# Performance work log

Hardware: AMD Instinct MI355X
Metric: run time of the kernel (lower is better)

Reference implementation:

```python
import jax, jax.numpy as jnp
import numpy as np
from jax import lax

B, T, D, H, W = 2, 8, 64, 64, 64
E, HID = 4, 256


def _layernorm(x, g, b, eps=1e-5):
    m = x.mean(-1, keepdims=True)
    v = ((x - m) ** 2).mean(-1, keepdims=True)
    return (x - m) / jnp.sqrt(v + eps) * g + b


def _pscan(A, X, axis):
    # linear recurrence h_t = A_t * h_{t-1} + X_t via associative scan
    def comb(l, r):
        a1, x1 = l
        a2, x2 = r
        return a2 * a1, a2 * x1 + x2
    return lax.associative_scan(comb, (A, X), axis=axis)[1]


def setup_inputs() -> dict:
    key = jax.random.key(0)
    ks = jax.random.split(key, 32)
    r = lambda i, shape, s=1.0: jax.random.normal(ks[i], shape, jnp.float32) * s
    D2 = 2 * D
    return {
        'x_re': r(0, (B, T, D, H, W)), 'x_im': r(1, (B, T, D, H, W)),
        'dt': jax.random.uniform(ks[2], (T,), jnp.float32, 0.5, 1.0),
        'ln_s_g': jnp.ones(D2), 'ln_s_b': jnp.zeros(D2),
        'conv_w': r(3, (3, 3, D2, D2), 0.03), 'conv_b': jnp.zeros(D2),
        'mom_w': r(4, (D2, D2), 0.08), 'mom_b': jnp.zeros(D2),
        'adv_w': jnp.full((1,), 0.1, jnp.float32),
        'enc_re': r(5, (D, D), 0.1), 'enc_im': r(6, (D, D), 0.1),
        'dec_re': r(7, (D, D), 0.1), 'dec_im': r(8, (D, D), 0.1),
        'flux_a_re': r(9, (D,)), 'flux_a_im': r(10, (D,), 0.1),
        'fin_re': r(11, (D, D), 0.1), 'fin_im': r(12, (D, D), 0.1),
        'fproj_re': r(13, (D, D), 0.1), 'fproj_im': r(14, (D, D), 0.1),
        'gate_w': r(15, (D2, D), 0.1), 'gate_b': jnp.zeros(D),
        'lam_re': r(16, (D,)), 'lam_im': r(17, (D,), 0.1),
        'noise_re': r(18, (B, T, H, W, D)), 'noise_im': r(19, (B, T, H, W, D)),
        'e_scale': jnp.full((1,), 0.1, jnp.float32),
        'ln_t_g': jnp.ones(D2), 'ln_t_b': jnp.zeros(D2),
        'router_w': r(20, (D2, E), 0.1), 'router_b': jnp.zeros(E),
        'w1': r(21, (E, D2, HID), 0.08), 'b1': jnp.zeros((E, HID)),
        'w2': r(22, (E, HID, D2), 0.08), 'b2': jnp.zeros((E, D2)),
    }


def _forward(x_re, x_im, dt, ln_s_g, ln_s_b, conv_w, conv_b, mom_w, mom_b, adv_w,
             enc_re, enc_im, dec_re, dec_im, flux_a_re, flux_a_im, fin_re, fin_im,
             fproj_re, fproj_im, gate_w, gate_b, lam_re, lam_im, noise_re, noise_im,
             e_scale, ln_t_g, ln_t_b, router_w, router_b, w1, b1, w2, b2):
    x = (x_re + 1j * x_im).astype(jnp.complex64)            # [B,T,D,H,W]
    target_energy = (jnp.abs(x) ** 2).mean(axis=(-2, -1))   # [B,T,D]
    momentum = x.mean(axis=(-2, -1))                        # [B,T,D] complex
    xcl = jnp.transpose(x, (0, 1, 3, 4, 2))                 # [B,T,H,W,D]
    Bs, Ts, Hs, Ws, Ds = xcl.shape
    D2 = 2 * Ds
    # --- spatial complex (Clifford) conv branch: LN over 2D channels + conv ---
    xr = jnp.concatenate([xcl.real, xcl.imag], -1)          # [B,T,H,W,2D]
    xn = _layernorm(xr, ln_s_g, ln_s_b)
    y = lax.conv_general_dilated(xn.reshape(Bs * Ts, Hs, Ws, D2), conv_w,
                                 (1, 1), 'SAME',
                                 dimension_numbers=('NHWC', 'HWIO', 'NHWC')) + conv_b
    y = y.reshape(Bs, Ts, Hs, Ws, D2)
    xcl = xcl + (y[..., :Ds] + 1j * y[..., Ds:])
    # --- momentum advection ---
    z_mean = xcl.mean(axis=(2, 3))                          # [B,T,D]
    mom_cat = jnp.concatenate([momentum.real, momentum.imag], -1) @ mom_w + mom_b
    mom_new = mom_cat[..., :Ds] + 1j * mom_cat[..., Ds:]
    dtb = jnp.broadcast_to(dt[None, :], (Bs, Ts))
    xcl = xcl + (mom_new * adv_w[0])[:, :, None, None, :] * dtb[:, :, None, None, None]
    momentum = 0.9 * momentum + 0.1 * z_mean
    # --- eigenbasis encode ---
    x_eigen = xcl @ (enc_re + 1j * enc_im)                  # [B,T,H,W,D]
    x_mean = x_eigen.mean(axis=(2, 3))                      # [B,T,D]
    # --- flux tracker: parallel scan over T ---
    A_flux = jnp.exp(-jax.nn.softplus(flux_a_re) + 1j * flux_a_im)
    A_flux = jnp.broadcast_to(A_flux, (Bs, Ts, Ds)).astype(jnp.complex64)
    X_flux = x_mean @ (fin_re + 1j * fin_im)
    flux_seq = _pscan(A_flux, X_flux, axis=1)               # [B,T,D]
    source = flux_seq @ (fproj_re + 1j * fproj_im)
    gate = jax.nn.sigmoid(jnp.concatenate([flux_seq.real, flux_seq.imag], -1) @ gate_w + gate_b)
    g = gate[:, :, None, None, :]
    forcing = x_eigen * g + source[:, :, None, None, :] * (1.0 - g)
    # --- temporal propagation: per-site parallel scan over T ---
    lam = -jax.nn.softplus(lam_re) + 1j * lam_im            # [D]
    op_decay = jnp.exp(lam[None, None, :] * dtb[:, :, None])  # [B,T,D]
    op_forcing = (op_decay - 1.0) / lam
    u_t = forcing * op_forcing[:, :, None, None, :]
    A_time = jnp.broadcast_to(op_decay[:, :, None, None, :], u_t.shape)
    u_out = _pscan(A_time, u_t, axis=1)                     # [B,T,H,W,D]
    noise = 0.01 * jnp.sqrt(dtb)[:, :, None, None, None] * (noise_re + 1j * noise_im)
    u_out = u_out + noise
    # --- decode + energy projection ---
    x_out = u_out @ (dec_re + 1j * dec_im)                  # [B,T,H,W,D]
    cur_e = (jnp.abs(x_out) ** 2).mean(axis=(2, 3))
    ratio = jnp.clip(target_energy / (cur_e + 1e-8), 0.5, 2.0)
    sf = jnp.sqrt(ratio)[:, :, None, None, :]
    x_out = x_out * (1.0 + e_scale[0] * (sf - 1.0))
    # --- temporal LN + MoE FFN on real-concat tokens ---
    xr2 = jnp.concatenate([x_out.real, x_out.imag], -1)
    xn2 = _layernorm(xr2, ln_t_g, ln_t_b)                   # [B,T,H,W,2D]
    tok = xn2.reshape(-1, D2)                               # [N,2D]
    p = jax.nn.softmax(tok @ router_w + router_b, -1)       # [N,E]
    hmid = jax.nn.gelu(jnp.einsum('nd,edh->neh', tok, w1) + b1)
    eout = jnp.einsum('neh,ehd->ned', hmid, w2) + b2
    out_tok = tok + jnp.einsum('ne,ned->nd', p, eout)
    out = out_tok.reshape(Bs, Ts, Hs, Ws, D2)
    x_out_c = out[..., :Ds] + 1j * out[..., Ds:]
    z_out = xcl + x_out_c
    z = jnp.transpose(z_out, (0, 1, 4, 2, 3))               # [B,T,D,H,W]
    return jnp.stack([z.real, z.imag])                      # [2,B,T,D,H,W]


def reference(x_re, x_im, dt, ln_s_g, ln_s_b, conv_w, conv_b, mom_w, mom_b, adv_w,
              enc_re, enc_im, dec_re, dec_im, flux_a_re, flux_a_im, fin_re, fin_im,
              fproj_re, fproj_im, gate_w, gate_b, lam_re, lam_im, noise_re, noise_im,
              e_scale, ln_t_g, ln_t_b, router_w, router_b, w1, b1, w2, b2):
    return _forward(x_re, x_im, dt, ln_s_g, ln_s_b, conv_w, conv_b, mom_w, mom_b, adv_w,
                    enc_re, enc_im, dec_re, dec_im, flux_a_re, flux_a_im, fin_re, fin_im,
                    fproj_re, fproj_im, gate_w, gate_b, lam_re, lam_im, noise_re, noise_im,
                    e_scale, ln_t_g, ln_t_b, router_w, router_b, w1, b1, w2, b2)
```

## Files before the change

### kernel.cpp

```cpp
#include <hip/hip_runtime.h>
#include <hip/hip_bf16.h>
#include <math.h>


#define W_XCL_RE 0u
#define W_XCL_IM 4194304u
#define W_C      8388608u
#define W_CWT    12582912u
#define W_W1T    14680064u
#define W_W2T    14745600u
#define W_ENCM   14811136u
#define W_DECM   14819328u
#define W_XMP_RE 14827520u
#define W_XMP_IM 14893056u
#define W_EP_RE  14958592u
#define W_EP_IM  15220736u
#define W_EIG_RE 16777216u
#define W_EIG_IM 20971520u
#define W_K1R    16777216u
#define W_K1I    16842752u
#define W_K1E    16908288u
#define W_SMALL  25165824u
#define W_TE     (W_SMALL+0u)
#define W_MOMRE  (W_SMALL+1024u)
#define W_MOMIM  (W_SMALL+2048u)
#define W_MTRE   (W_SMALL+3072u)
#define W_MTIM   (W_SMALL+4096u)
#define W_GATE   (W_SMALL+5120u)
#define W_SRCRE  (W_SMALL+6144u)
#define W_SRCIM  (W_SMALL+7168u)
#define W_OPFRE  (W_SMALL+8192u)
#define W_OPFIM  (W_SMALL+9216u)
#define W_OPDRE  (W_SMALL+10240u)
#define W_OPDIM  (W_SMALL+11264u)
#define W_SCALE  (W_SMALL+12288u)

typedef __attribute__((ext_vector_type(8))) short bf16x8;
typedef __attribute__((ext_vector_type(4))) float f32x4;

__device__ __forceinline__ unsigned short bfr(float x) {
  __hip_bfloat16 h = __float2bfloat16(x);
  return *(unsigned short*)&h;
}
__device__ __forceinline__ unsigned int pk2(float a, float b) {
  return ((unsigned int)bfr(b) << 16) | (unsigned int)bfr(a);
}

__global__ __launch_bounds__(256) void k2_transpose_ln(
    const float* __restrict__ xre, const float* __restrict__ xim,
    const float* __restrict__ g, const float* __restrict__ bb_, float* ws) {
  int blk = blockIdx.x; int bt = blk >> 6, h = blk & 63;
  __shared__ float tre[64][65], tim[64][65];
  __shared__ float ps[4][64], pq[4][64], pe[4][64];
  __shared__ float mean_l[64], rstd_l[64];
  size_t inbase = (size_t)bt * 262144 + (size_t)h * 64;
  for (int i = threadIdx.x; i < 1024; i += 256) {
    int d = i >> 4, w4 = (i & 15) * 4;
    float4 vr = *(const float4*)&xre[inbase + (size_t)d * 4096 + w4];
    float4 vi = *(const float4*)&xim[inbase + (size_t)d * 4096 + w4];
    tre[d][w4] = vr.x; tre[d][w4 + 1] = vr.y; tre[d][w4 + 2] = vr.z; tre[d][w4 + 3] = vr.w;
    tim[d][w4] = vi.x; tim[d][w4 + 1] = vi.y; tim[d][w4 + 2] = vi.z; tim[d][w4 + 3] = vi.w;
  }
  __syncthreads();
  {
    int w = threadIdx.x & 63, part = threadIdx.x >> 6;
    float s = 0.f, sq = 0.f;
    for (int dd = part * 16; dd < part * 16 + 16; dd++) {
      float vr = tre[dd][w], vi = tim[dd][w];
      s += vr + vi; sq += vr * vr + vi * vi;
    }
    ps[part][w] = s; pq[part][w] = sq;
  }
  __syncthreads();
  if (threadIdx.x < 64) {
    int w = threadIdx.x;
    float s  = ps[0][w] + ps[1][w] + ps[2][w] + ps[3][w];
    float sq = pq[0][w] + pq[1][w] + pq[2][w] + pq[3][w];
    float m = s / 128.f;
    float v = sq / 128.f - m * m;
    mean_l[w] = m; rstd_l[w] = rsqrtf(v + 1e-5f);
  }
  __syncthreads();
  {
    int d = threadIdx.x & 63, part = threadIdx.x >> 6;
    float sr = 0.f, si = 0.f, se = 0.f;
    for (int w = part * 16; w < part * 16 + 16; w++) {
      float vr = tre[d][w], vi = tim[d][w];
      sr += vr; si += vi; se += vr * vr + vi * vi;
    }
    ps[part][d] = sr; pq[part][d] = si; pe[part][d] = se;
  }
  __syncthreads();
  if (threadIdx.x < 64) {
    int d = threadIdx.x;
    int idx = h * 1024 + bt * 64 + d;
    ws[W_K1R + idx] = ps[0][d] + ps[1][d] + ps[2][d] + ps[3][d];
    ws[W_K1I + idx] = pq[0][d] + pq[1][d] + pq[2][d] + pq[3][d];
    ws[W_K1E + idx] = pe[0][d] + pe[1][d] + pe[2][d] + pe[3][d];
  }
  size_t tokbase = (size_t)blk * 64;
  for (int i = threadIdx.x; i < 1024; i += 256) {
    int w = i >> 4, d4 = (i & 15) * 4;
    float4 o, p;
    o.x = tre[d4][w]; o.y = tre[d4 + 1][w]; o.z = tre[d4 + 2][w]; o.w = tre[d4 + 3][w];
    p.x = tim[d4][w]; p.y = tim[d4 + 1][w]; p.z = tim[d4 + 2][w]; p.w = tim[d4 + 3][w];
    *(float4*)&ws[W_XCL_RE + tokbase * 64 + (size_t)w * 64 + d4] = o;
    *(float4*)&ws[W_XCL_IM + tokbase * 64 + (size_t)w * 64 + d4] = p;
  }
  __hip_bfloat16* xnb = (__hip_bfloat16*)(ws + W_C);
  int c0 = (threadIdx.x & 63) * 2, wg = threadIdx.x >> 6;
  float gc0 = g[c0], bc0 = bb_[c0], gc1 = g[c0 + 1], bc1 = bb_[c0 + 1];
  for (int pass = 0; pass < 16; pass++) {
    int w = pass * 4 + wg;
    float m = mean_l[w], rs = rstd_l[w];
    float v0 = (c0 < 64) ? tre[c0][w] : tim[c0 - 64][w];
    float v1 = (c0 + 1 < 64) ? tre[c0 + 1][w] : tim[c0 + 1 - 64][w];
    *(unsigned int*)&xnb[tokbase * 128 + (size_t)w * 128 + c0] =
        pk2((v0 - m) * rs * gc0 + bc0, (v1 - m) * rs * gc1 + bc1);
  }
}

__global__ void k1b_finish(float* ws) {
  int bt = blockIdx.x, d = threadIdx.x;
  float a = 0.f, b = 0.f, c = 0.f;
  for (int h = 0; h < 64; h++) {
    int idx = h * 1024 + bt * 64 + d;
    a += ws[W_K1R + idx]; b += ws[W_K1I + idx]; c += ws[W_K1E + idx];
  }
  ws[W_MOMRE + bt * 64 + d] = a / 4096.f;
  ws[W_MOMIM + bt * 64 + d] = b / 4096.f;
  ws[W_TE + bt * 64 + d]    = c / 4096.f;
}

__global__ void k2b_mom(const float* __restrict__ mom_w, const float* __restrict__ mom_b,
                        const float* __restrict__ adv_w, const float* __restrict__ dt, float* ws) {
  int bt = blockIdx.x; int t = bt & 7;
  __shared__ float mc[128], outl[128];
  int tid = threadIdx.x;
  mc[tid] = (tid < 64) ? ws[W_MOMRE + bt * 64 + tid] : ws[W_MOMIM + bt * 64 + tid - 64];
  __syncthreads();
  float acc = mom_b[tid];
  for (int k = 0; k < 128; k++) acc += mc[k] * mom_w[k * 128 + tid];
  outl[tid] = acc;
  __syncthreads();
  if (tid < 64) {
    float f = adv_w[0] * dt[t];
    ws[W_MTRE + bt * 64 + tid] = outl[tid] * f;
    ws[W_MTIM + bt * 64 + tid] = outl[64 + tid] * f;
  }
}

__global__ void k0_wprep(const float* __restrict__ w1, const float* __restrict__ w2,
                         const float* __restrict__ cw,
                         const float* __restrict__ enc_re, const float* __restrict__ enc_im,
                         const float* __restrict__ dec_re, const float* __restrict__ dec_im,
                         float* ws) {
  __hip_bfloat16* w1f = (__hip_bfloat16*)(ws + W_W1T);
  __hip_bfloat16* w2f = (__hip_bfloat16*)(ws + W_W2T);
  __hip_bfloat16* cwt = (__hip_bfloat16*)(ws + W_CWT);
  __hip_bfloat16* encM = (__hip_bfloat16*)(ws + W_ENCM);
  __hip_bfloat16* decM = (__hip_bfloat16*)(ws + W_DECM);
  int idx = blockIdx.x * 256 + threadIdx.x;
  if (idx < 131072) {
    {
      int j = idx & 7, lane = (idx >> 3) & 63, kt = (idx >> 9) & 3, nt = (idx >> 11) & 15, e = idx >> 15;
      int cout = nt * 16 + (lane & 15);
      int cin = kt * 32 + (lane >> 4) * 8 + j;
      w1f[idx] = __float2bfloat16(w1[((size_t)(e * 128 + cin)) * 256 + cout]);
    }
    {
      int j = idx & 7, lane = (idx >> 3) & 63, kt = (idx >> 9) & 7, nt = (idx >> 12) & 7, e = idx >> 15;
      int cout = nt * 16 + (lane & 15);
      int cin = kt * 32 + (lane >> 4) * 8 + j;
      w2f[idx] = __float2bfloat16(w2[((size_t)(e * 256 + cin)) * 128 + cout]);
    }
  }
  if (idx < 147456) {
    int j = idx & 7, lane = (idx >> 3) & 63, kt = (idx >> 9) & 3, r = idx >> 11;
    int nt = r & 7, tap = r >> 3;
    int cout = nt * 16 + (lane & 15);
    int cin = kt * 32 + (lane >> 4) * 8 + j;
    cwt[idx] = __float2bfloat16(cw[((size_t)(tap * 128 + cin)) * 128 + cout]);
  }
  if (idx < 16384) {
    int jj = idx & 7, lane = (idx >> 3) & 63, kt = (idx >> 9) & 3, nt = idx >> 11;
    int jc = nt * 16 + (lane & 15);
    int k = kt * 32 + (lane >> 4) * 8 + jj;
    float ve, vd;
    if (k < 64) {
      ve = (jc < 64) ? enc_re[k * 64 + jc] : enc_im[k * 64 + (jc - 64)];
      vd = (jc < 64) ? dec_re[k * 64 + jc] : dec_im[k * 64 + (jc - 64)];
    } else {
      int kk = k - 64;
      ve = (jc < 64) ? -enc_im[kk * 64 + jc] : enc_re[kk * 64 + (jc - 64)];
      vd = (jc < 64) ? -dec_im[kk * 64 + jc] : dec_re[kk * 64 + (jc - 64)];
    }
    encM[idx] = __float2bfloat16(ve);
    decM[idx] = __float2bfloat16(vd);
  }
}

__global__ __launch_bounds__(256) void k3_conv_enc(const float* __restrict__ cb, float* ws) {
  int blk = blockIdx.x; int bt = blk >> 6, h = blk & 63;
  const __hip_bfloat16* xnb = (const __hip_bfloat16*)(ws + W_C);
  const __hip_bfloat16* cwt = (const __hip_bfloat16*)(ws + W_CWT);
  const __hip_bfloat16* encM = (const __hip_bfloat16*)(ws + W_ENCM);
  __shared__ __align__(16) char smem[3 * 66 * 136 * 2];
  __hip_bfloat16 (*xin)[66][136] = (__hip_bfloat16(*)[66][136])smem;
  char* A = smem;
  int tid = threadIdx.x, lane = tid & 63, wv = tid >> 6;
  int arow = lane & 15, kgrp = (lane >> 4) * 8, rbase = (lane >> 4) * 4;

  for (int r = 0; r < 3; r++) {
    int hh = h + r - 1;
    if (hh < 0 || hh >= 64) {
      unsigned int* z = (unsigned int*)&xin[r][0][0];
      for (int i = tid; i < 4488; i += 256) z[i] = 0u;
    } else {
      if (tid < 68) *(unsigned int*)&xin[r][0][tid * 2] = 0u;
      else if (tid < 136) *(unsigned int*)&xin[r][65][(tid - 136 + 68) * 2] = 0u;
      const __hip_bfloat16* src = xnb + ((size_t)bt * 4096 + (size_t)hh * 64) * 128;
      for (int i = tid; i < 1024; i += 256) {
        int wp = (i >> 4) + 1, c8 = (i & 15) * 8;
        *(bf16x8*)&xin[r][wp][c8] = *(const bf16x8*)&src[(size_t)(wp - 1) * 128 + c8];
      }
    }
  }
  __syncthreads();

  f32x4 oacc[4][2];
  #pragma unroll
  for (int m = 0; m < 4; m++) {
    oacc[m][0] = (f32x4){0.f, 0.f, 0.f, 0.f};
    oacc[m][1] = (f32x4){0.f, 0.f, 0.f, 0.f};
  }

  for (int tap = 0; tap < 9; tap++) {
    int kh = tap / 3, kw = tap % 3;
    const __hip_bfloat16* wt0 = cwt + ((size_t)(tap * 8 + wv * 2) * 4) * 512 + lane * 8;
    #pragma unroll
    for (int kt = 0; kt < 4; kt++) {
      bf16x8 a[4];
      #pragma unroll
      for (int m = 0; m < 4; m++)
        a[m] = *(const bf16x8*)&xin[kh][m * 16 + arow + kw][kt * 32 + kgrp];
      bf16x8 b0 = *(const bf16x8*)&wt0[(size_t)kt * 512];
      bf16x8 b1 = *(const bf16x8*)&wt0[(size_t)(kt + 4) * 512];
      #pragma unroll
      for (int m = 0; m < 4; m++) {
        oacc[m][0] = __builtin_amdgcn_mfma_f32_16x16x32_bf16(a[m], b0, oacc[m][0], 0, 0, 0);
        oacc[m][1] = __builtin_amdgcn_mfma_f32_16x16x32_bf16(a[m], b1, oacc[m][1], 0, 0, 0);
      }
    }
  }
  __syncthreads();

  size_t rowtok = (size_t)blk * 64;
  #pragma unroll
  for (int n = 0; n < 2; n++) {
    int cout = (wv * 2 + n) * 16 + arow;
    bool isre = cout < 64;
    int d = cout & 63;
    float add = cb[cout] + ws[(isre ? W_MTRE : W_MTIM) + bt * 64 + d];
    float* xcl = ws + (isre ? W_XCL_RE : W_XCL_IM);
    #pragma unroll
    for (int m = 0; m < 4; m++)
      #pragma unroll
      for (int r = 0; r < 4; r++) {
        int w = m * 16 + rbase + r;
        float v = xcl[(rowtok + w) * 64 + d] + oacc[m][n][r] + add;
        xcl[(rowtok + w) * 64 + d] = v;
        *(__hip_bfloat16*)(A + w * 256 + ((cout * 2) ^ ((w & 7) << 4))) = __float2bfloat16(v);
      }
  }
  __syncthreads();

  f32x4 acc[4][2];
  #pragma unroll
  for (int m = 0; m < 4; m++) {
    acc[m][0] = (f32x4){0.f, 0.f, 0.f, 0.f};
    acc[m][1] = (f32x4){0.f, 0.f, 0.f, 0.f};
  }
  #pragma unroll
  for (int kt = 0; kt < 4; kt++) {
    bf16x8 a[4];
    #pragma unroll
    for (int m = 0; m < 4; m++)
      a[m] = *(const bf16x8*)(A + (m * 16 + arow) * 256 + (((kt * 32 + kgrp) * 2) ^ ((arow & 7) << 4)));
    bf16x8 b0 = *(const bf16x8*)&encM[(((size_t)(wv * 2 + 0) * 4 + kt) * 64 + lane) * 8];
    bf16x8 b1 = *(const bf16x8*)&encM[(((size_t)(wv * 2 + 1) * 4 + kt) * 64 + lane) * 8];
    #pragma unroll
    for (int m = 0; m < 4; m++) {
      acc[m][0] = __builtin_amdgcn_mfma_f32_16x16x32_bf16(a[m], b0, acc[m][0], 0, 0, 0);
      acc[m][1] = __builtin_amdgcn_mfma_f32_16x16x32_bf16(a[m], b1, acc[m][1], 0, 0, 0);
    }
  }
  float* orp = ws + W_EIG_RE;
  float* oip = ws + W_EIG_IM;
  #pragma unroll
  for (int n = 0; n < 2; n++) {
    int jc = (wv * 2 + n) * 16 + arow;
    float* dst = (jc < 64) ? orp : oip;
    int col = jc & 63;
    #pragma unroll
    for (int m = 0; m < 4; m++)
      #pragma unroll
      for (int r = 0; r < 4; r++)
        dst[(rowtok + m * 16 + rbase + r) * 64 + col] = acc[m][n][r];
    float s = 0.f;
    #pragma unroll
    for (int m = 0; m < 4; m++)
      #pragma unroll
      for (int r = 0; r < 4; r++) s += acc[m][n][r];
    s += __shfl_xor(s, 16);
    s += __shfl_xor(s, 32);
    if (lane < 16)
      ws[(jc < 64 ? W_XMP_RE : W_XMP_IM) + (size_t)blk * 64 + col] = s;
  }
}

__device__ __forceinline__ float softplusf(float x) {
  return (x > 20.f) ? x : log1pf(expf(x));
}

__global__ void k6_seq(const float* __restrict__ fin_re, const float* __restrict__ fin_im,
                       const float* __restrict__ fproj_re, const float* __restrict__ fproj_im,
                       const float* __restrict__ flux_a_re, const float* __restrict__ flux_a_im,
                       const float* __restrict__ gate_w, const float* __restrict__ gate_b,
                       const float* __restrict__ lam_re, const float* __restrict__ lam_im,
                       const float* __restrict__ dt, float* ws) {
  __shared__ float xmr[1024], xmi[1024], Xfr[1024], Xfi[1024], flr[1024], fli[1024];
  int tid = threadIdx.x;
  for (int i = tid; i < 1024; i += 256) {
    int bt = i >> 6, j = i & 63;
    float sr = 0.f, si = 0.f;
    for (int q = 0; q < 64; q++) {
      sr += ws[W_XMP_RE + (size_t)(bt * 64 + q) * 64 + j];
      si += ws[W_XMP_IM + (size_t)(bt * 64 + q) * 64 + j];
    }
    xmr[i] = sr / 4096.f; xmi[i] = si / 4096.f;
  }
  __syncthreads();
  for (int i = tid; i < 1024; i += 256) {
    int bt = i >> 6, j = i & 63;
    float ar = 0.f, ai = 0.f;
    for (int d = 0; d < 64; d++) {
      float xr = xmr[bt * 64 + d], xi = xmi[bt * 64 + d];
      float wr = fin_re[d * 64 + j], wi = fin_im[d * 64 + j];
      ar += xr * wr - xi * wi; ai += xr * wi + xi * wr;
    }
    Xfr[i] = ar; Xfi[i] = ai;
  }
  __syncthreads();
  if (tid < 128) {
    int b = tid >> 6, j = tid & 63;
    float mag = expf(-softplusf(flux_a_re[j]));
    float aar = mag * cosf(flux_a_im[j]), aai = mag * sinf(flux_a_im[j]);
    float sr = 0.f, si = 0.f;
    for (int t = 0; t < 8; t++) {
      int idx = (b * 8 + t) * 64 + j;
      float nr = aar * sr - aai * si + Xfr[idx];
      float ni = aar * si + aai * sr + Xfi[idx];
      sr = nr; si = ni;
      flr[idx] = sr; fli[idx] = si;
    }
  }
  __syncthreads();
  for (int i = tid; i < 1024; i += 256) {
    int bt = i >> 6, j = i & 63;
    float ar = 0.f, ai = 0.f, lg = 0.f;
    for (int d = 0; d < 64; d++) {
      float fr = flr[bt * 64 + d], fi = fli[bt * 64 + d];
      float wr = fproj_re[d * 64 + j], wi = fproj_im[d * 64 + j];
      ar += fr * wr - fi * wi; ai += fr * wi + fi * wr;
      lg += fr * gate_w[d * 64 + j] + fi * gate_w[(64 + d) * 64 + j];
    }
    ws[W_SRCRE + i] = ar; ws[W_SRCIM + i] = ai;
    ws[W_GATE + i] = 1.f / (1.f + expf(-(lg + gate_b[j])));
  }
  for (int i = tid; i < 1024; i += 256) {
    int bt = i >> 6, d = i & 63, t = bt & 7;
    float lr = -softplusf(lam_re[d]), li = lam_im[d];
    float dtv = dt[t];
    float mag = expf(lr * dtv);
    float dr = mag * cosf(li * dtv), di = mag * sinf(li * dtv);
    ws[W_OPDRE + i] = dr; ws[W_OPDIM + i] = di;
    float omr = dr - 1.f, omi = di;
    float den = lr * lr + li * li;
    ws[W_OPFRE + i] = (omr * lr + omi * li) / den;
    ws[W_OPFIM + i] = (omi * lr - omr * li) / den;
  }
}

__global__ __launch_bounds__(256) void k7_dec(const float* __restrict__ nre,
                                              const float* __restrict__ nim,
                                              const float* __restrict__ dt, float* ws) {
  int blk = blockIdx.x;
  int b = blk >> 8, h = (blk >> 2) & 63, wq = blk & 3;
  const __hip_bfloat16* decM = (const __hip_bfloat16*)(ws + W_DECM);
  __shared__ float gl[8][64], srl[8][64], sil[8][64], ofr[8][64], ofi[8][64], odr[8][64], odi[8][64];
  __shared__ __align__(16) char A[4096];
  __shared__ float dts[8];
  int tid = threadIdx.x, lane = tid & 63, wv = tid >> 6;
  int arow = lane & 15, kgrp = (lane >> 4) * 8, rbase = (lane >> 4) * 4;
  for (int i = tid; i < 512; i += 256) {
    int t = i >> 6, d = i & 63, idx = (b * 8 + t) * 64 + d;
    gl[t][d]  = ws[W_GATE + idx];
    srl[t][d] = ws[W_SRCRE + idx]; sil[t][d] = ws[W_SRCIM + idx];
    ofr[t][d] = ws[W_OPFRE + idx]; ofi[t][d] = ws[W_OPFIM + idx];
    odr[t][d] = ws[W_OPDRE + idx]; odi[t][d] = ws[W_OPDIM + idx];
  }
  if (tid < 8) dts[tid] = dt[tid];
  __syncthreads();

  int d = tid & 63, wbase = tid >> 6;
  float ur[4], ui[4];
  #pragma unroll
  for (int k = 0; k < 4; k++) { ur[k] = 0.f; ui[k] = 0.f; }

  for (int t = 0; t < 8; t++) {
    float ns = 0.01f * sqrtf(dts[t]);
    size_t tokb = ((size_t)(b * 8 + t) * 64 + h) * 64 + (size_t)wq * 16;
    #pragma unroll
    for (int k = 0; k < 4; k++) {
      int wl = wbase + 4 * k;
      size_t off = (tokb + wl) * 64 + d;
      float er_ = ws[W_EIG_RE + off], ei_ = ws[W_EIG_IM + off];
      float gg = gl[t][d];
      float fre = er_ * gg + srl[t][d] * (1.f - gg);
      float fim = ei_ * gg + sil[t][d] * (1.f - gg);
      float utr = fre * ofr[t][d] - fim * ofi[t][d];
      float uti = fre * ofi[t][d] + fim * ofr[t][d];
      float nur = odr[t][d] * ur[k] - odi[t][d] * ui[k] + utr;
      float nui = odr[t][d] * ui[k] + odi[t][d] * ur[k] + uti;
      ur[k] = nur; ui[k] = nui;
      float uor = nur + ns * nre[off];
      float uoi = nui + ns * nim[off];
      int sw = (wl & 7) << 4;
      *(__hip_bfloat16*)(A + wl * 256 + ((d * 2) ^ sw)) = __float2bfloat16(uor);
      *(__hip_bfloat16*)(A + wl * 256 + (((64 + d) * 2) ^ sw)) = __float2bfloat16(uoi);
    }
    __syncthreads();
    f32x4 acc[2];
    acc[0] = (f32x4){0.f, 0.f, 0.f, 0.f};
    acc[1] = (f32x4){0.f, 0.f, 0.f, 0.f};
    #pragma unroll
    for (int kt = 0; kt < 4; kt++) {
      bf16x8 a0 = *(const bf16x8*)(A + arow * 256 + (((kt * 32 + kgrp) * 2) ^ ((arow & 7) << 4)));
      bf16x8 b0 = *(const bf16x8*)&decM[(((size_t)(wv * 2 + 0) * 4 + kt) * 64 + lane) * 8];
      bf16x8 b1 = *(const bf16x8*)&decM[(((size_t)(wv * 2 + 1) * 4 + kt) * 64 + lane) * 8];
      acc[0] = __builtin_amdgcn_mfma_f32_16x16x32_bf16(a0, b0, acc[0], 0, 0, 0);
      acc[1] = __builtin_amdgcn_mfma_f32_16x16x32_bf16(a0, b1, acc[1], 0, 0, 0);
    }
    float* orp = ws + W_EIG_RE;
    float* oip = ws + W_EIG_IM;
    #pragma unroll
    for (int n = 0; n < 2; n++) {
      int jc = (wv * 2 + n) * 16 + arow;
      float* dst = (jc < 64) ? orp : oip;
      int col = jc & 63;
      #pragma unroll
      for (int r = 0; r < 4; r++)
        dst[(tokb + rbase + r) * 64 + col] = acc[n][r];
      float s = acc[n][0] * acc[n][0] + acc[n][1] * acc[n][1]
              + acc[n][2] * acc[n][2] + acc[n][3] * acc[n][3];
      s += __shfl_xor(s, 16);
      s += __shfl_xor(s, 32);
      if (lane < 16)
        ws[(jc < 64 ? W_EP_RE : W_EP_IM)
           + (size_t)((b * 8 + t) * 256 + h * 4 + wq) * 64 + col] = s;
    }
    __syncthreads();
  }
}

__global__ void k9b_scale(const float* __restrict__ escale, float* ws) {
  int bt = blockIdx.x; int j = threadIdx.x;
  float s = 0.f;
  for (int q = 0; q < 256; q++) {
    size_t idx = (size_t)(bt * 256 + q) * 64 + j;
    s += ws[W_EP_RE + idx] + ws[W_EP_IM + idx];
  }
  float cur = s / 4096.f;
  float te = ws[W_TE + bt * 64 + j];
  float ratio = te / (cur + 1e-8f);
  ratio = fminf(fmaxf(ratio, 0.5f), 2.0f);
  ws[W_SCALE + bt * 64 + j] = 1.f + escale[0] * (sqrtf(ratio) - 1.f);
}

__global__ __launch_bounds__(512) void k11_moe(
    const float* __restrict__ rw, const float* __restrict__ rb,
    const float* __restrict__ b1, const float* __restrict__ b2,
    const float* __restrict__ g2, const float* __restrict__ b2_,
    float* __restrict__ ws, float* __restrict__ out) {
  int blk = blockIdx.x; int bt = blk >> 6, h = blk & 63;
  const __hip_bfloat16* w1f = (const __hip_bfloat16*)(ws + W_W1T);
  const __hip_bfloat16* w2f = (const __hip_bfloat16*)(ws + W_W2T);
  __shared__ __align__(16) char smem[49152];
  __shared__ float pl[64][4];
  __shared__ float sc[64];
  __shared__ float mean_l[64], rstd_l[64];
  char* lt = smem;
  char* hb = smem + 16384;
  float (*obuf)[129] = (float(*)[129])smem;
  float* psq = (float*)(smem + 16384);
  int tid = threadIdx.x, lane = tid & 63, wv = tid >> 6;
  int arow = lane & 15, kgrp = (lane >> 4) * 8, rbase = (lane >> 4) * 4;
  size_t tokbase = (size_t)blk * 64;

  if (tid < 64) sc[tid] = ws[W_SCALE + bt * 64 + tid];
  __syncthreads();

  int w = tid >> 3, part = tid & 7;
  int c0 = part * 16, dbase = (part & 3) * 16;
  const float* rowp = ws + ((part < 4) ? W_EIG_RE : W_EIG_IM) + (tokbase + w) * 64 + dbase;
  float4 vv[4];
  {
    float s = 0.f, sq = 0.f;
    #pragma unroll
    for (int q = 0; q < 4; q++) {
      float4 t4 = *(const float4*)&rowp[q * 4];
      t4.x *= sc[dbase + q * 4 + 0];
      t4.y *= sc[dbase + q * 4 + 1];
      t4.z *= sc[dbase + q * 4 + 2];
      t4.w *= sc[dbase + q * 4 + 3];
      vv[q] = t4;
      s  += t4.x + t4.y + t4.z + t4.w;
      sq += t4.x * t4.x + t4.y * t4.y + t4.z * t4.z + t4.w * t4.w;
    }
    psq[part * 64 + w] = s;
    psq[512 + part * 64 + w] = sq;
  }
  __syncthreads();
  if (tid < 64) {
    float s = 0.f, sq = 0.f;
    #pragma unroll
    for (int p = 0; p < 8; p++) { s += psq[p * 64 + tid]; sq += psq[512 + p * 64 + tid]; }
    float m = s / 128.f, v = sq / 128.f - m * m;
    mean_l[tid] = m; rstd_l[tid] = rsqrtf(v + 1e-5f);
  }
  __syncthreads();
  {
    float m = mean_l[w], rs = rstd_l[w];
    int szw = (w & 7) << 4;
    #pragma unroll
    for (int q = 0; q < 4; q++) {
      int c = c0 + q * 4;
      float a0 = (vv[q].x - m) * rs * g2[c]     + b2_[c];
      float a1 = (vv[q].y - m) * rs * g2[c + 1] + b2_[c + 1];
      float a2 = (vv[q].z - m) * rs * g2[c + 2] + b2_[c + 2];
      float a3 = (vv[q].w - m) * rs * g2[c + 3] + b2_[c + 3];
      *(unsigned int*)(lt + w * 256 + ((c * 2) ^ szw)) = pk2(a0, a1);
      *(unsigned int*)(lt + w * 256 + (((c + 2) * 2) ^ szw)) = pk2(a2, a3);
    }
  }
  __syncthreads();
  if (tid < 256) {
    int l = tid >> 2, e = tid & 3;
    float acc = rb[e];
    const float* rwe = rw + e;
    int sz = (l & 7) << 4;
    for (int dd = 0; dd < 128; dd += 2) {
      unsigned int u = *(const unsigned int*)(lt + l * 256 + ((dd * 2) ^ sz));
      float x0 = __uint_as_float(u << 16);
      float x1 = __uint_as_float(u & 0xffff0000u);
      acc += x0 * rwe[dd * 4] + x1 * rwe[dd * 4 + 4];
    }
    pl[l][e] = acc;
  }
  __syncthreads();
  if (tid < 64) {
    float m = fmaxf(fmaxf(pl[tid][0], pl[tid][1]), fmaxf(pl[tid][2], pl[tid][3]));
    float e0 = expf(pl[tid][0] - m), e1 = expf(pl[tid][1] - m);
    float e2 = expf(pl[tid][2] - m), e3 = expf(pl[tid][3] - m);
    float s = e0 + e1 + e2 + e3;
    float rs = __builtin_amdgcn_rcpf(s);
    pl[tid][0] = e0 * rs; pl[tid][1] = e1 * rs; pl[tid][2] = e2 * rs; pl[tid][3] = e3 * rs;
  }

  f32x4 oacc[4];
  #pragma unroll
  for (int m = 0; m < 4; m++) {
    int col = wv * 16 + arow;
    oacc[m] = (f32x4){0.f, 0.f, 0.f, 0.f};
    #pragma unroll
    for (int r = 0; r < 4; r++) {
      int row = m * 16 + rbase + r;
      oacc[m][r] = __bfloat162float(
          *(const __hip_bfloat16*)(lt + row * 256 + ((col * 2) ^ ((row & 7) << 4))));
    }
  }
  __syncthreads();

  for (int e = 0; e < 4; e++) {
    f32x4 acc1[4][2];
    #pragma unroll
    for (int m = 0; m < 4; m++) {
      acc1[m][0] = (f32x4){0.f, 0.f, 0.f, 0.f};
      acc1[m][1] = (f32x4){0.f, 0.f, 0.f, 0.f};
    }
    #pragma unroll
    for (int kt = 0; kt < 4; kt++) {
      bf16x8 a[4];
      #pragma unroll
      for (int m = 0; m < 4; m++) {
        int row = m * 16 + arow;
        a[m] = *(const bf16x8*)(lt + row * 256 + (((kt * 32 + kgrp) * 2) ^ ((arow & 7) << 4)));
      }
      bf16x8 b0 = *(const bf16x8*)&w1f[(((size_t)(e * 16 + wv * 2 + 0) * 4 + kt) * 64 + lane) * 8];
      bf16x8 b1 = *(const bf16x8*)&w1f[(((size_t)(e * 16 + wv * 2 + 1) * 4 + kt) * 64 + lane) * 8];
      #pragma unroll
      for (int m = 0; m < 4; m++) {
        acc1[m][0] = __builtin_amdgcn_mfma_f32_16x16x32_bf16(a[m], b0, acc1[m][0], 0, 0, 0);
        acc1[m][1] = __builtin_amdgcn_mfma_f32_16x16x32_bf16(a[m], b1, acc1[m][1], 0, 0, 0);
      }
    }
    __syncthreads();
    #pragma unroll
    for (int n = 0; n < 2; n++) {
      int col = (wv * 2 + n) * 16 + arow;
      float bv = b1[e * 256 + col];
      #pragma unroll
      for (int m = 0; m < 4; m++)
        #pragma unroll
        for (int r = 0; r < 4; r++) {
          float hv = acc1[m][n][r] + bv;
          float z = 1.5957691216f * hv + 0.0713548162f * hv * hv * hv;
          float gelu = hv * __builtin_amdgcn_rcpf(1.f + __expf(-z));
          int row = m * 16 + rbase + r;
          *(__hip_bfloat16*)(hb + row * 512 + ((col * 2) ^ ((row & 7) << 4))) =
              __float2bfloat16(gelu);
        }
    }
    __syncthreads();
    f32x4 acc2[4];
    #pragma unroll
    for (int m = 0; m < 4; m++) acc2[m] = (f32x4){0.f, 0.f, 0.f, 0.f};
    #pragma unroll
    for (int kt = 0; kt < 8; kt++) {
      bf16x8 a2[4];
      #pragma unroll
      for (int m = 0; m < 4; m++) {
        int row = m * 16 + arow;
        a2[m] = *(const bf16x8*)(hb + row * 512 + (((kt * 32 + kgrp) * 2) ^ ((arow & 7) << 4)));
      }
      bf16x8 bb = *(const bf16x8*)&w2f[(((size_t)(e * 8 + wv) * 8 + kt) * 64 + lane) * 8];
      #pragma unroll
      for (int m = 0; m < 4; m++)
        acc2[m] = __builtin_amdgcn_mfma_f32_16x16x32_bf16(a2[m], bb, acc2[m], 0, 0, 0);
    }
    {
      int col = wv * 16 + arow;
      float bv2 = b2[e * 128 + col];
      #pragma unroll
      for (int m = 0; m < 4; m++)
        #pragma unroll
        for (int r = 0; r < 4; r++)
          oacc[m][r] += pl[m * 16 + rbase + r][e] * (acc2[m][r] + bv2);
    }
  }

  __syncthreads();
  #pragma unroll
  for (int m = 0; m < 4; m++) {
    int col = wv * 16 + arow;
    #pragma unroll
    for (int r = 0; r < 4; r++)
      obuf[m * 16 + rbase + r][col] = oacc[m][r];
  }
  __syncthreads();

  {
    const float* xre = ws + W_XCL_RE;
    const float* xim = ws + W_XCL_IM;
    for (int i = tid; i < 8192; i += 512) {
      int wt = i >> 7, c = i & 127, dd = c & 63;
      float val = ((c < 64) ? xre : xim)[(tokbase + wt) * 64 + dd];
      obuf[wt][c] += val;
    }
  }
  __syncthreads();
  for (int i = tid; i < 8192; i += 512) {
    int d2 = i >> 6, wt = i & 63;
    out[(size_t)(d2 >> 6) * 4194304 + (size_t)bt * 262144 + (size_t)(d2 & 63) * 4096
        + (size_t)h * 64 + wt] = obuf[wt][d2];
  }
}

extern "C" void kernel_launch(void* const* d_in, const int* in_sizes, int n_in,
                              void* d_out, int out_size, void* d_ws, size_t ws_size,
                              hipStream_t stream) {
  const float* x_re      = (const float*)d_in[0];
  const float* x_im      = (const float*)d_in[1];
  const float* dt        = (const float*)d_in[2];
  const float* ln_s_g    = (const float*)d_in[3];
  const float* ln_s_b    = (const float*)d_in[4];
  const float* conv_w    = (const float*)d_in[5];
  const float* conv_b    = (const float*)d_in[6];
  const float* mom_w     = (const float*)d_in[7];
  const float* mom_b     = (const float*)d_in[8];
  const float* adv_w     = (const float*)d_in[9];
  const float* enc_re    = (const float*)d_in[10];
  const float* enc_im    = (const float*)d_in[11];
  const float* dec_re    = (const float*)d_in[12];
  const float* dec_im    = (const float*)d_in[13];
  const float* flux_a_re = (const float*)d_in[14];
  const float* flux_a_im = (const float*)d_in[15];
  const float* fin_re    = (const float*)d_in[16];
  const float* fin_im    = (const float*)d_in[17];
  const float* fproj_re  = (const float*)d_in[18];
  const float* fproj_im  = (const float*)d_in[19];
  const float* gate_w    = (const float*)d_in[20];
  const float* gate_b    = (const float*)d_in[21];
  const float* lam_re    = (const float*)d_in[22];
  const float* lam_im    = (const float*)d_in[23];
  const float* noise_re  = (const float*)d_in[24];
  const float* noise_im  = (const float*)d_in[25];
  const float* e_scale   = (const float*)d_in[26];
  const float* ln_t_g    = (const float*)d_in[27];
  const float* ln_t_b    = (const float*)d_in[28];
  const float* router_w  = (const float*)d_in[29];
  const float* router_b  = (const float*)d_in[30];
  const float* w1        = (const float*)d_in[31];
  const float* b1        = (const float*)d_in[32];
  const float* w2        = (const float*)d_in[33];
  const float* b2        = (const float*)d_in[34];
  float* ws  = (float*)d_ws;
  float* out = (float*)d_out;

  k0_wprep<<<576, 256, 0, stream>>>(w1, w2, conv_w, enc_re, enc_im, dec_re, dec_im, ws);
  k2_transpose_ln<<<1024, 256, 0, stream>>>(x_re, x_im, ln_s_g, ln_s_b, ws);
  k1b_finish<<<16, 64, 0, stream>>>(ws);
  k2b_mom<<<16, 128, 0, stream>>>(mom_w, mom_b, adv_w, dt, ws);
  k3_conv_enc<<<1024, 256, 0, stream>>>(conv_b, ws);
  k6_seq<<<1, 256, 0, stream>>>(fin_re, fin_im, fproj_re, fproj_im, flux_a_re, flux_a_im,
                                gate_w, gate_b, lam_re, lam_im, dt, ws);
  k7_dec<<<512, 256, 0, stream>>>(noise_re, noise_im, dt, ws);
  k9b_scale<<<16, 64, 0, stream>>>(e_scale, ws);
  k11_moe<<<1024, 512, 0, stream>>>(router_w, router_b, b1, b2, ln_t_g, ln_t_b, ws, out);
}
```

Baseline: 269.4 us.

## Split MoE hidden dimension into halves to shrink LDS and vectorize epilogue I/O

The MoE kernel now computes the expert hidden layer in two 128-wide halves, running GELU and the second GEMM on each half in turn. This halves the hidden-activation LDS buffer (49152 down to 33280 bytes) and the acc1 register footprint, which should allow more blocks per CU. In exchange it adds an extra pair of barriers per expert. The residual-add and the final output store are also changed to use float4 global loads and stores.

```diff
diff --git a/kernel.cpp b/kernel.cpp
--- a/kernel.cpp
+++ b/kernel.cpp
@@ -496,7 +496,7 @@
   int blk = blockIdx.x; int bt = blk >> 6, h = blk & 63;
   const __hip_bfloat16* w1f = (const __hip_bfloat16*)(ws + W_W1T);
   const __hip_bfloat16* w2f = (const __hip_bfloat16*)(ws + W_W2T);
-  __shared__ __align__(16) char smem[49152];
+  __shared__ __align__(16) char smem[33280];
   __shared__ float pl[64][4];
   __shared__ float sc[64];
   __shared__ float mean_l[64], rstd_l[64];
@@ -593,61 +593,58 @@
   __syncthreads();
 
   for (int e = 0; e < 4; e++) {
-    f32x4 acc1[4][2];
-    #pragma unroll
-    for (int m = 0; m < 4; m++) {
-      acc1[m][0] = (f32x4){0.f, 0.f, 0.f, 0.f};
-      acc1[m][1] = (f32x4){0.f, 0.f, 0.f, 0.f};
-    }
-    #pragma unroll
-    for (int kt = 0; kt < 4; kt++) {
-      bf16x8 a[4];
-      #pragma unroll
-      for (int m = 0; m < 4; m++) {
-        int row = m * 16 + arow;
-        a[m] = *(const bf16x8*)(lt + row * 256 + (((kt * 32 + kgrp) * 2) ^ ((arow & 7) << 4)));
+    f32x4 acc2[4];
+    #pragma unroll
+    for (int m = 0; m < 4; m++) acc2[m] = (f32x4){0.f, 0.f, 0.f, 0.f};
+    #pragma unroll
+    for (int hh = 0; hh < 2; hh++) {
+      f32x4 acc1[4];
+      #pragma unroll
+      for (int m = 0; m < 4; m++) acc1[m] = (f32x4){0.f, 0.f, 0.f, 0.f};
+      #pragma unroll
+      for (int kt = 0; kt < 4; kt++) {
+        bf16x8 a[4];
+        #pragma unroll
+        for (int m = 0; m < 4; m++) {
+          int row = m * 16 + arow;
+          a[m] = *(const bf16x8*)(lt + row * 256 + (((kt * 32 + kgrp) * 2) ^ ((arow & 7) << 4)));
+        }
+        bf16x8 b0 = *(const bf16x8*)&w1f[(((size_t)(e * 16 + hh * 8 + wv) * 4 + kt) * 64 + lane) * 8];
+        #pragma unroll
+        for (int m = 0; m < 4; m++)
+          acc1[m] = __builtin_amdgcn_mfma_f32_16x16x32_bf16(a[m], b0, acc1[m], 0, 0, 0);
       }
-      bf16x8 b0 = *(const bf16x8*)&w1f[(((size_t)(e * 16 + wv * 2 + 0) * 4 + kt) * 64 + lane) * 8];
-      bf16x8 b1 = *(const bf16x8*)&w1f[(((size_t)(e * 16 + wv * 2 + 1) * 4 + kt) * 64 + lane) * 8];
-      #pragma unroll
-      for (int m = 0; m < 4; m++) {
-        acc1[m][0] = __builtin_amdgcn_mfma_f32_16x16x32_bf16(a[m], b0, acc1[m][0], 0, 0, 0);
-        acc1[m][1] = __builtin_amdgcn_mfma_f32_16x16x32_bf16(a[m], b1, acc1[m][1], 0, 0, 0);
+      __syncthreads();
+      {
+        int colh = wv * 16 + arow;
+        float bv = b1[e * 256 + hh * 128 + colh];
+        #pragma unroll
+        for (int m = 0; m < 4; m++)
+          #pragma unroll
+          for (int r = 0; r < 4; r++) {
+            float hv = acc1[m][r] + bv;
+            float z = 1.5957691216f * hv + 0.0713548162f * hv * hv * hv;
+            float gelu = hv * __builtin_amdgcn_rcpf(1.f + __expf(-z));
+            int row = m * 16 + rbase + r;
+            *(__hip_bfloat16*)(hb + row * 256 + ((colh * 2) ^ ((row & 7) << 4))) =
+                __float2bfloat16(gelu);
+          }
       }
-    }
-    __syncthreads();
-    #pragma unroll
-    for (int n = 0; n < 2; n++) {
-      int col = (wv * 2 + n) * 16 + arow;
-      float bv = b1[e * 256 + col];
-      #pragma unroll
-      for (int m = 0; m < 4; m++)
+      __syncthreads();
+      #pragma unroll
+      for (int kt2 = 0; kt2 < 4; kt2++) {
+        bf16x8 a2[4];
         #pragma unroll
-        for (int r = 0; r < 4; r++) {
-          float hv = acc1[m][n][r] + bv;
-          float z = 1.5957691216f * hv + 0.0713548162f * hv * hv * hv;
-          float gelu = hv * __builtin_amdgcn_rcpf(1.f + __expf(-z));
-          int row = m * 16 + rbase + r;
-          *(__hip_bfloat16*)(hb + row * 512 + ((col * 2) ^ ((row & 7) << 4))) =
-              __float2bfloat16(gelu);
+        for (int m = 0; m < 4; m++) {
+          int row = m * 16 + arow;
+          a2[m] = *(const bf16x8*)(hb + row * 256 + (((kt2 * 32 + kgrp) * 2) ^ ((arow & 7) << 4)));
         }
-    }
-    __syncthreads();
-    f32x4 acc2[4];
-    #pragma unroll
-    for (int m = 0; m < 4; m++) acc2[m] = (f32x4){0.f, 0.f, 0.f, 0.f};
-    #pragma unroll
-    for (int kt = 0; kt < 8; kt++) {
-      bf16x8 a2[4];
-      #pragma unroll
-      for (int m = 0; m < 4; m++) {
-        int row = m * 16 + arow;
-        a2[m] = *(const bf16x8*)(hb + row * 512 + (((kt * 32 + kgrp) * 2) ^ ((arow & 7) << 4)));
+        int ktg = hh * 4 + kt2;
+        bf16x8 bb = *(const bf16x8*)&w2f[(((size_t)(e * 8 + wv) * 8 + ktg) * 64 + lane) * 8];
+        #pragma unroll
+        for (int m = 0; m < 4; m++)
+          acc2[m] = __builtin_amdgcn_mfma_f32_16x16x32_bf16(a2[m], bb, acc2[m], 0, 0, 0);
       }
-      bf16x8 bb = *(const bf16x8*)&w2f[(((size_t)(e * 8 + wv) * 8 + kt) * 64 + lane) * 8];
-      #pragma unroll
-      for (int m = 0; m < 4; m++)
-        acc2[m] = __builtin_amdgcn_mfma_f32_16x16x32_bf16(a2[m], bb, acc2[m], 0, 0, 0);
     }
     {
       int col = wv * 16 + arow;
@@ -673,17 +670,23 @@
   {
     const float* xre = ws + W_XCL_RE;
     const float* xim = ws + W_XCL_IM;
-    for (int i = tid; i < 8192; i += 512) {
-      int wt = i >> 7, c = i & 127, dd = c & 63;
-      float val = ((c < 64) ? xre : xim)[(tokbase + wt) * 64 + dd];
-      obuf[wt][c] += val;
-    }
-  }
-  __syncthreads();
-  for (int i = tid; i < 8192; i += 512) {
-    int d2 = i >> 6, wt = i & 63;
-    out[(size_t)(d2 >> 6) * 4194304 + (size_t)bt * 262144 + (size_t)(d2 & 63) * 4096
-        + (size_t)h * 64 + wt] = obuf[wt][d2];
+    for (int i = tid; i < 2048; i += 512) {
+      int wt = i >> 5, c4 = (i & 31) * 4;
+      const float* src = (c4 < 64) ? &xre[(tokbase + wt) * 64 + c4]
+                                   : &xim[(tokbase + wt) * 64 + (c4 - 64)];
+      float4 v = *(const float4*)src;
+      obuf[wt][c4] += v.x; obuf[wt][c4 + 1] += v.y;
+      obuf[wt][c4 + 2] += v.z; obuf[wt][c4 + 3] += v.w;
+    }
+  }
+  __syncthreads();
+  for (int i = tid; i < 2048; i += 512) {
+    int d2 = i >> 4, wt4 = (i & 15) * 4;
+    float4 v;
+    v.x = obuf[wt4][d2]; v.y = obuf[wt4 + 1][d2];
+    v.z = obuf[wt4 + 2][d2]; v.w = obuf[wt4 + 3][d2];
+    *(float4*)&out[(size_t)(d2 >> 6) * 4194304 + (size_t)bt * 262144
+                   + (size_t)(d2 & 63) * 4096 + (size_t)h * 64 + wt4] = v;
   }
 }
 
```

Result: no change. 274.4 us (+1.9%).
